# Kernel tuning notes

Measured on AMD Instinct MI355X. Metric: run time of the kernel, lower is better.

## Reference

```python
import jax, jax.numpy as jnp
import numpy as np

N_NODES, N_EDGES, N_GRAPHS = 50000, 800000, 128
D_IN, D_DEG, D_H, D_OUT, MAX_DEG = 32, 32, 64, 32, 128
D0 = D_IN + D_DEG + 1  # 65 = node_input_dim
N_GIN = 5  # num_layers - 1


def setup_inputs() -> dict:
    key = jax.random.key(0)
    ks = jax.random.split(key, 20)
    lin = lambda k, i, o: (jax.random.normal(k, (i, o), jnp.float32) / np.sqrt(i)).astype(jnp.float32)
    inp = {
        "x": jax.random.normal(ks[0], (N_NODES, D_IN), jnp.float32),
        "edge_index": jax.random.randint(ks[1], (2, N_EDGES), 0, N_NODES, jnp.int32),
        "batch": jnp.sort(jax.random.randint(ks[2], (N_NODES,), 0, N_GRAPHS, jnp.int32)),
        "root_n_id": jax.random.randint(ks[3], (N_GRAPHS,), 0, N_NODES, jnp.int32),
        "deg_table": 0.1 * jax.random.normal(ks[4], (MAX_DEG + 1, D_DEG), jnp.float32),
        # GIN layer 0 MLP (input dim 65), layers 1..4 (input dim 64), each MLP has 2 linears
        "w1_0": lin(ks[5], D0, D_H), "b1_0": 0.01 * jax.random.normal(ks[6], (D_H,), jnp.float32),
        "w2_0": lin(ks[7], D_H, D_H), "b2_0": 0.01 * jax.random.normal(ks[8], (D_H,), jnp.float32),
        "w1_rest": jnp.stack([lin(jax.random.fold_in(ks[9], i), D_H, D_H) for i in range(N_GIN - 1)]),
        "b1_rest": 0.01 * jax.random.normal(ks[10], (N_GIN - 1, D_H), jnp.float32),
        "w2_rest": jnp.stack([lin(jax.random.fold_in(ks[11], i), D_H, D_H) for i in range(N_GIN - 1)]),
        "b2_rest": 0.01 * jax.random.normal(ks[12], (N_GIN - 1, D_H), jnp.float32),
        # 3 BatchNorms per GIN layer: MLP-hidden BN, ApplyNodeFunc BN, outer BN
        "bn_gamma": 1.0 + 0.1 * jax.random.normal(ks[13], (N_GIN, 3, D_H), jnp.float32),
        "bn_beta": 0.1 * jax.random.normal(ks[14], (N_GIN, 3, D_H), jnp.float32),
        # per-layer prediction heads (layer 0 sees raw n_feat of dim 65)
        "pred_w0": lin(ks[15], D0, D_OUT), "pred_b0": 0.01 * jax.random.normal(ks[16], (D_OUT,), jnp.float32),
        "pred_w_rest": jnp.stack([lin(jax.random.fold_in(ks[17], i), D_H, D_OUT) for i in range(N_GIN)]),
        "pred_b_rest": 0.01 * jax.random.normal(ks[18], (N_GIN, D_OUT), jnp.float32),
    }
    return inp


def _bn(h, g, b):
    # training-mode BatchNorm1d over the node axis (biased variance), eps=1e-5
    m = h.mean(axis=0)
    v = h.var(axis=0)
    return g * (h - m) * jax.lax.rsqrt(v + 1e-5) + b


def _forward(x, edge_index, batch, root_n_id, deg_table, w1_0, b1_0, w2_0, b2_0,
             w1_rest, b1_rest, w2_rest, b2_rest, bn_gamma, bn_beta,
             pred_w0, pred_b0, pred_w_rest, pred_b_rest):
    N = x.shape[0]
    G = root_n_id.shape[0]
    src, dst = edge_index[0], edge_index[1]

    # degree(edge_index[0]) clamped to max_degree, then embedded
    deg = jax.ops.segment_sum(jnp.ones_like(src), src, num_segments=N)
    deg = jnp.clip(deg, 0, deg_table.shape[0] - 1)
    ego = jnp.zeros((N, 1), x.dtype).at[root_n_id].set(1.0)
    h = jnp.concatenate([x, deg_table[deg], ego], axis=-1)  # [N, 65]

    w1s = [w1_0] + [w1_rest[i] for i in range(w1_rest.shape[0])]
    b1s = [b1_0] + [b1_rest[i] for i in range(b1_rest.shape[0])]
    w2s = [w2_0] + [w2_rest[i] for i in range(w2_rest.shape[0])]
    b2s = [b2_0] + [b2_rest[i] for i in range(b2_rest.shape[0])]

    hidden = [h]
    for l in range(len(w1s)):
        # GINConv, sum aggregation, eps = 0: (1+eps)*h + sum_{j in N(i)} h_j
        agg = jax.ops.segment_sum(h[src], dst, num_segments=N)  # [N, d]
        z = h + agg
        z = jax.nn.relu(_bn(z @ w1s[l] + b1s[l], bn_gamma[l, 0], bn_beta[l, 0]))  # MLP hidden
        z = z @ w2s[l] + b2s[l]                                                  # MLP out (linear)
        z = jax.nn.relu(_bn(z, bn_gamma[l, 1], bn_beta[l, 1]))                   # ApplyNodeFunc BN+ReLU
        z = jax.nn.relu(_bn(z, bn_gamma[l, 2], bn_beta[l, 2]))                   # outer BN+ReLU
        h = z
        hidden.append(h)

    pred_ws = [pred_w0] + [pred_w_rest[i] for i in range(pred_w_rest.shape[0])]
    pred_bs = [pred_b0] + [pred_b_rest[i] for i in range(pred_b_rest.shape[0])]
    score = jnp.zeros((G, pred_w0.shape[1]), x.dtype)
    for i, hi in enumerate(hidden):
        pooled = jax.ops.segment_sum(hi, batch, num_segments=G)  # global_add_pool
        score = score + pooled @ pred_ws[i] + pred_bs[i]         # dropout is identity in eval
    # F.normalize(p=2, eps=1e-5)
    nrm = jnp.maximum(jnp.linalg.norm(score, axis=-1, keepdims=True), 1e-5)
    return score / nrm


def reference(x, edge_index, batch, root_n_id, deg_table, w1_0, b1_0, w2_0, b2_0,
              w1_rest, b1_rest, w2_rest, b2_rest, bn_gamma, bn_beta,
              pred_w0, pred_b0, pred_w_rest, pred_b_rest):
    return _forward(x, edge_index, batch, root_n_id, deg_table, w1_0, b1_0, w2_0, b2_0,
                    w1_rest, b1_rest, w2_rest, b2_rest, bn_gamma, bn_beta,
                    pred_w0, pred_b0, pred_w_rest, pred_b_rest)
```

## Files before the change

### kernel.cpp

```cpp
#include <hip/hip_runtime.h>

#define PAD 8
#define NREP 16
#define CHUNK 64

#define BCAST(v, l) __uint_as_float(__builtin_amdgcn_readlane(__float_as_uint(v), (l)))

__global__ __launch_bounds__(256) void count_k(const int* __restrict__ src,
    const int* __restrict__ dst, int* __restrict__ deg, int* __restrict__ cnt, int E) {
  int e = blockIdx.x * 256 + threadIdx.x;
  if (e < E) {
    atomicAdd(&deg[src[e] * PAD], 1);
    atomicAdd(&cnt[dst[e] * PAD], 1);
  }
}

__global__ __launch_bounds__(256) void scan1_k(const int* __restrict__ cnt,
    int* __restrict__ off, int* __restrict__ bsum, int N) {
  __shared__ int s[256];
  int t = threadIdx.x;
  int i = blockIdx.x * 256 + t;
  int c = (i < N) ? cnt[i * PAD] : 0;
  s[t] = c;
  __syncthreads();
  for (int d = 1; d < 256; d <<= 1) {
    int v = (t >= d) ? s[t - d] : 0;
    __syncthreads();
    s[t] += v;
    __syncthreads();
  }
  if (i < N) off[i + 1] = s[t];
  if (t == 255) bsum[blockIdx.x] = s[255];
}

__global__ __launch_bounds__(256) void scan2_k(int* __restrict__ bsum, int NB) {
  __shared__ int s[256];
  int t = threadIdx.x;
  int c = (t < NB) ? bsum[t] : 0;
  s[t] = c;
  __syncthreads();
  for (int d = 1; d < 256; d <<= 1) {
    int v = (t >= d) ? s[t - d] : 0;
    __syncthreads();
    s[t] += v;
    __syncthreads();
  }
  if (t < NB) bsum[t] = s[t] - c;
}

__global__ __launch_bounds__(256) void scan3_k(int* __restrict__ off,
    const int* __restrict__ bsum, int N) {
  int i = blockIdx.x * 256 + threadIdx.x;
  if (i < N) off[i + 1] += bsum[blockIdx.x];
  if (i == 0) off[0] = 0;
}

__global__ __launch_bounds__(256) void fill_k(const int* __restrict__ src,
    const int* __restrict__ dst, const int* __restrict__ off,
    int* __restrict__ cnt, int* __restrict__ csr, int E) {
  int e = blockIdx.x * 256 + threadIdx.x;
  if (e < E) {
    int d = dst[e];
    int old = atomicSub(&cnt[d * PAD], 1);
    csr[off[d + 1] - old] = src[e];
  }
}

__global__ void root_k(const int* __restrict__ root, int* __restrict__ egof, int G) {
  int g = threadIdx.x;
  if (g < G) egof[root[g]] = 1;
}

__global__ __launch_bounds__(256) void h0_k(const float* __restrict__ x,
    const float* __restrict__ deg_table, const int* __restrict__ deg,
    const int* __restrict__ egof, const int* __restrict__ batch,
    float* __restrict__ h0, float* __restrict__ pool0, int N) {
  int w = threadIdx.x >> 6, f = threadIdx.x & 63;
  int base = blockIdx.x * CHUNK;
  int end = min(base + CHUNK, N);
  float accum = 0.0f, accum64 = 0.0f;
  int curg = -1;
  for (int n0 = base + w; n0 < end; n0 += 4) {
    int n = __builtin_amdgcn_readfirstlane(n0);
    float v;
    if (f < 32) {
      v = x[n * 32 + f];
    } else {
      int d = deg[n * PAD];
      if (d > 128) d = 128;
      v = deg_table[d * 32 + (f - 32)];
    }
    h0[(size_t)n * 72 + f] = v;
    float e = 0.0f;
    if (f == 0) {
      e = egof[n] ? 1.0f : 0.0f;
      h0[(size_t)n * 72 + 64] = e;
    }
    int g = batch[n];
    if (g != curg) {
      if (curg >= 0) {
        atomicAdd(&pool0[curg * 72 + f], accum);
        if (f == 0 && accum64 != 0.0f) atomicAdd(&pool0[curg * 72 + 64], accum64);
      }
      curg = g;
      accum = v;
      accum64 = e;
    } else {
      accum += v;
      accum64 += e;
    }
  }
  if (curg >= 0) {
    atomicAdd(&pool0[curg * 72 + f], accum);
    if (f == 0 && accum64 != 0.0f) atomicAdd(&pool0[curg * 72 + 64], accum64);
  }
}

template <int FEATS, int STRIDE>
__global__ __launch_bounds__(256) void layer1_k(const float* __restrict__ h,
    const int* __restrict__ off, const int* __restrict__ csr,
    const float* __restrict__ W1, const float* __restrict__ B1,
    float* __restrict__ z1, float* __restrict__ sums, int N) {
  __shared__ float Wsh[FEATS * 64];
  __shared__ float ls[256], lq[256];
  const int t = threadIdx.x;
  for (int i = t; i < FEATS * 64; i += 256) Wsh[i] = W1[i];
  __syncthreads();
  const int w = t >> 6, lane = t & 63;
  const float bj = B1[lane];
  float s = 0.0f, q = 0.0f;
  const int step = gridDim.x * 4;
  for (int n0 = blockIdx.x * 4 + w; n0 < N; n0 += step) {
    const int n = __builtin_amdgcn_readfirstlane(n0);
    const float* row = h + (size_t)n * STRIDE;
    float z = row[lane];
    float z64 = 0.0f;
    if (FEATS == 65) { if (lane == 0) z64 = row[64]; }
    const int k1 = off[n + 1];
    int k = off[n];
    for (; k + 8 <= k1; k += 8) {
      int i0 = csr[k], i1 = csr[k + 1], i2 = csr[k + 2], i3 = csr[k + 3];
      int i4 = csr[k + 4], i5 = csr[k + 5], i6 = csr[k + 6], i7 = csr[k + 7];
      const float* r0 = h + (size_t)i0 * STRIDE;
      const float* r1 = h + (size_t)i1 * STRIDE;
      const float* r2 = h + (size_t)i2 * STRIDE;
      const float* r3 = h + (size_t)i3 * STRIDE;
      const float* r4 = h + (size_t)i4 * STRIDE;
      const float* r5 = h + (size_t)i5 * STRIDE;
      const float* r6 = h + (size_t)i6 * STRIDE;
      const float* r7 = h + (size_t)i7 * STRIDE;
      float v0 = r0[lane], v1 = r1[lane], v2 = r2[lane], v3 = r3[lane];
      float v4 = r4[lane], v5 = r5[lane], v6 = r6[lane], v7 = r7[lane];
      if (FEATS == 65) {
        if (lane == 0)
          z64 += ((r0[64] + r1[64]) + (r2[64] + r3[64])) +
                 ((r4[64] + r5[64]) + (r6[64] + r7[64]));
      }
      z += ((v0 + v1) + (v2 + v3)) + ((v4 + v5) + (v6 + v7));
    }
    for (; k < k1; k++) {
      const float* r0 = h + (size_t)csr[k] * STRIDE;
      z += r0[lane];
      if (FEATS == 65) { if (lane == 0) z64 += r0[64]; }
    }
    float a0 = bj, a1 = 0.0f, a2 = 0.0f, a3 = 0.0f;
#pragma unroll
    for (int k2 = 0; k2 < 64; k2 += 4) {
      a0 += BCAST(z, k2) * Wsh[k2 * 64 + lane];
      a1 += BCAST(z, k2 + 1) * Wsh[(k2 + 1) * 64 + lane];
      a2 += BCAST(z, k2 + 2) * Wsh[(k2 + 2) * 64 + lane];
      a3 += BCAST(z, k2 + 3) * Wsh[(k2 + 3) * 64 + lane];
    }
    if (FEATS == 65) a0 += BCAST(z64, 0) * Wsh[64 * 64 + lane];
    float acc = (a0 + a1) + (a2 + a3);
    z1[(size_t)n * 64 + lane] = acc;
    s += acc;
    q += acc * acc;
  }
  ls[t] = s; lq[t] = q;
  __syncthreads();
  if (t < 64) {
    float a = ls[t] + ls[64 + t] + ls[128 + t] + ls[192 + t];
    atomicAdd(&sums[(blockIdx.x & (NREP - 1)) * 128 + t], a);
  } else if (t < 128) {
    int f = t - 64;
    float a = lq[f] + lq[64 + f] + lq[128 + f] + lq[192 + f];
    atomicAdd(&sums[(blockIdx.x & (NREP - 1)) * 128 + 64 + f], a);
  }
}

__global__ __launch_bounds__(256) void layer2_k(const float* __restrict__ z1,
    const float* __restrict__ W2, const float* __restrict__ B2,
    const float* __restrict__ sums0, const float* __restrict__ g0,
    const float* __restrict__ be0, float invN,
    float* __restrict__ z2, float* __restrict__ sums1, int N) {
  __shared__ float Wsh[64 * 64];
  __shared__ float redu[128];
  __shared__ float scs[64], shs[64];
  __shared__ float ls[256], lq[256];
  const int t = threadIdx.x;
  for (int i = t; i < 64 * 64; i += 256) Wsh[i] = W2[i];
  if (t < 128) {
    float a = 0.0f;
#pragma unroll
    for (int b = 0; b < NREP; b++) a += sums0[b * 128 + t];
    redu[t] = a;
  }
  __syncthreads();
  if (t < 64) {
    float m = redu[t] * invN;
    float var = redu[64 + t] * invN - m * m;
    float sc = g0[t] * rsqrtf(var + 1e-5f);
    scs[t] = sc;
    shs[t] = be0[t] - m * sc;
  }
  __syncthreads();
  const int w = t >> 6, lane = t & 63;
  const float sc = scs[lane], sh = shs[lane];
  const float bj = B2[lane];
  float s = 0.0f, q = 0.0f;
  const int step = gridDim.x * 4;
  for (int n0 = blockIdx.x * 4 + w; n0 < N; n0 += step) {
    const int n = __builtin_amdgcn_readfirstlane(n0);
    float v = z1[(size_t)n * 64 + lane];
    v = fmaxf(v * sc + sh, 0.0f);
    float a0 = bj, a1 = 0.0f, a2 = 0.0f, a3 = 0.0f;
#pragma unroll
    for (int k2 = 0; k2 < 64; k2 += 4) {
      a0 += BCAST(v, k2) * Wsh[k2 * 64 + lane];
      a1 += BCAST(v, k2 + 1) * Wsh[(k2 + 1) * 64 + lane];
      a2 += BCAST(v, k2 + 2) * Wsh[(k2 + 2) * 64 + lane];
      a3 += BCAST(v, k2 + 3) * Wsh[(k2 + 3) * 64 + lane];
    }
    float acc = (a0 + a1) + (a2 + a3);
    z2[(size_t)n * 64 + lane] = acc;
    s += acc;
    q += acc * acc;
  }
  ls[t] = s; lq[t] = q;
  __syncthreads();
  if (t < 64) {
    float a = ls[t] + ls[64 + t] + ls[128 + t] + ls[192 + t];
    atomicAdd(&sums1[(blockIdx.x & (NREP - 1)) * 128 + t], a);
  } else if (t < 128) {
    int f = t - 64;
    float a = lq[f] + lq[64 + f] + lq[128 + f] + lq[192 + f];
    atomicAdd(&sums1[(blockIdx.x & (NREP - 1)) * 128 + 64 + f], a);
  }
}

__global__ __launch_bounds__(256) void statsbn_k(const float* __restrict__ z2,
    const float* __restrict__ sums1, const float* __restrict__ g1,
    const float* __restrict__ be1, float invN, float* __restrict__ sums2, int N) {
  __shared__ float redu[128];
  __shared__ float scs[64], shs[64];
  __shared__ float ls[256], lq[256];
  int t = threadIdx.x;
  if (t < 128) {
    float a = 0.0f;
#pragma unroll
    for (int b = 0; b < NREP; b++) a += sums1[b * 128 + t];
    redu[t] = a;
  }
  __syncthreads();
  if (t < 64) {
    float m = redu[t] * invN;
    float var = redu[64 + t] * invN - m * m;
    float sc = g1[t] * rsqrtf(var + 1e-5f);
    scs[t] = sc;
    shs[t] = be1[t] - m * sc;
  }
  __syncthreads();
  int f = t & 63, r = t >> 6;
  float sc = scs[f], sh = shs[f];
  float s = 0.0f, q = 0.0f;
  for (int n = blockIdx.x * 4 + r; n < N; n += gridDim.x * 4) {
    float v = z2[(size_t)n * 64 + f];
    v = fmaxf(v * sc + sh, 0.0f);
    s += v;
    q += v * v;
  }
  ls[t] = s; lq[t] = q;
  __syncthreads();
  if (t < 64) {
    float a = ls[t] + ls[64 + t] + ls[128 + t] + ls[192 + t];
    atomicAdd(&sums2[(blockIdx.x & (NREP - 1)) * 128 + t], a);
  } else if (t < 128) {
    int ff = t - 64;
    float a = lq[ff] + lq[64 + ff] + lq[128 + ff] + lq[192 + ff];
    atomicAdd(&sums2[(blockIdx.x & (NREP - 1)) * 128 + 64 + ff], a);
  }
}

__global__ __launch_bounds__(256) void apply_k(const float* __restrict__ z2,
    const float* __restrict__ sums1, const float* __restrict__ g1, const float* __restrict__ be1,
    const float* __restrict__ sums2, const float* __restrict__ g2, const float* __restrict__ be2,
    float invN, const int* __restrict__ batch, float* __restrict__ hout,
    float* __restrict__ pool, int N, int writeH) {
  __shared__ float red1[128], red2[128];
  __shared__ float sc1s[64], sh1s[64], sc2s[64], sh2s[64];
  int t = threadIdx.x;
  if (t < 128) {
    float a = 0.0f, c = 0.0f;
#pragma unroll
    for (int b = 0; b < NREP; b++) { a += sums1[b * 128 + t]; c += sums2[b * 128 + t]; }
    red1[t] = a;
    red2[t] = c;
  }
  __syncthreads();
  if (t < 64) {
    float m = red1[t] * invN;
    float var = red1[64 + t] * invN - m * m;
    float sc = g1[t] * rsqrtf(var + 1e-5f);
    sc1s[t] = sc;
    sh1s[t] = be1[t] - m * sc;
    m = red2[t] * invN;
    var = red2[64 + t] * invN - m * m;
    sc = g2[t] * rsqrtf(var + 1e-5f);
    sc2s[t] = sc;
    sh2s[t] = be2[t] - m * sc;
  }
  __syncthreads();
  int w = t >> 6, f = t & 63;
  float sc1 = sc1s[f], sh1 = sh1s[f], sc2 = sc2s[f], sh2 = sh2s[f];
  int base = blockIdx.x * CHUNK;
  int end = min(base + CHUNK, N);
  float accum = 0.0f;
  int curg = -1;
  for (int n0 = base + w; n0 < end; n0 += 4) {
    int n = __builtin_amdgcn_readfirstlane(n0);
    float v = z2[(size_t)n * 64 + f];
    v = fmaxf(v * sc1 + sh1, 0.0f);
    v = fmaxf(v * sc2 + sh2, 0.0f);
    if (writeH) hout[(size_t)n * 64 + f] = v;
    int g = batch[n];
    if (g != curg) {
      if (curg >= 0) atomicAdd(&pool[curg * 64 + f], accum);
      curg = g;
      accum = v;
    } else {
      accum += v;
    }
  }
  if (curg >= 0) atomicAdd(&pool[curg * 64 + f], accum);
}

__global__ __launch_bounds__(64) void prednorm_k(const float* __restrict__ pool0,
    const float* __restrict__ pools, const float* __restrict__ pw0,
    const float* __restrict__ pb0, const float* __restrict__ pwr,
    const float* __restrict__ pbr, float* __restrict__ out, int G) {
  int g = blockIdx.x;
  int j = threadIdx.x;
  float acc = 0.0f;
  if (j < 32) {
    acc = pb0[j];
    for (int k = 0; k < 65; k++) acc += pool0[g * 72 + k] * pw0[k * 32 + j];
    for (int l = 0; l < 5; l++) {
      acc += pbr[l * 32 + j];
      const float* pl = pools + (size_t)l * G * 64 + (size_t)g * 64;
      const float* wl = pwr + (size_t)l * 64 * 32;
      for (int k = 0; k < 64; k++) acc += pl[k] * wl[k * 32 + j];
    }
  }
  float s = acc * acc;
  for (int o = 16; o > 0; o >>= 1) s += __shfl_xor(s, o);
  float nrm = fmaxf(sqrtf(s), 1e-5f);
  if (j < 32) out[g * 32 + j] = acc / nrm;
}

extern "C" void kernel_launch(void* const* d_in, const int* in_sizes, int n_in,
                              void* d_out, int out_size, void* d_ws, size_t ws_size,
                              hipStream_t stream) {
  (void)n_in; (void)out_size; (void)ws_size;
  const float* x          = (const float*)d_in[0];
  const int*   edge_index = (const int*)d_in[1];
  const int*   batch      = (const int*)d_in[2];
  const int*   root       = (const int*)d_in[3];
  const float* deg_table  = (const float*)d_in[4];
  const float* w1_0       = (const float*)d_in[5];
  const float* b1_0       = (const float*)d_in[6];
  const float* w2_0       = (const float*)d_in[7];
  const float* b2_0       = (const float*)d_in[8];
  const float* w1_rest    = (const float*)d_in[9];
  const float* b1_rest    = (const float*)d_in[10];
  const float* w2_rest    = (const float*)d_in[11];
  const float* b2_rest    = (const float*)d_in[12];
  const float* bn_gamma   = (const float*)d_in[13];
  const float* bn_beta    = (const float*)d_in[14];
  const float* pred_w0    = (const float*)d_in[15];
  const float* pred_b0    = (const float*)d_in[16];
  const float* pred_w_rest = (const float*)d_in[17];
  const float* pred_b_rest = (const float*)d_in[18];

  const int N = in_sizes[0] / 32;
  const int E = in_sizes[1] / 2;
  const int G = in_sizes[3];
  const int* src = edge_index;
  const int* dst = edge_index + E;
  const float invN = 1.0f / N;

  char* w = (char*)d_ws;
  auto alloc = [&](size_t bytes) {
    char* p = w;
    w += (bytes + 255) & ~(size_t)255;
    return p;
  };
  int* d_deg  = (int*)alloc((size_t)N * PAD * 4);
  int* d_cnt  = (int*)alloc((size_t)N * PAD * 4);
  int* d_egof = (int*)alloc((size_t)N * 4);
  char* zero_int_end = w;
  int* d_off  = (int*)alloc((size_t)(N + 1) * 4);
  int* d_bsum = (int*)alloc(256 * 4);
  int* d_csr  = (int*)alloc((size_t)E * 4);
  float* fsums = (float*)alloc((size_t)15 * NREP * 128 * 4);
  float* fpool = (float*)alloc((size_t)(G * 72 + 5 * G * 64) * 4);
  char* zero_f_end = w;
  float* fh0 = (float*)alloc((size_t)N * 72 * 4);
  float* fB1 = (float*)alloc((size_t)N * 64 * 4);
  float* fB2 = (float*)alloc((size_t)N * 64 * 4);
  float* fB3 = (float*)alloc((size_t)N * 64 * 4);

  hipMemsetAsync(d_deg, 0, (size_t)(zero_int_end - (char*)d_deg), stream);
  hipMemsetAsync(fsums, 0, (size_t)(zero_f_end - (char*)fsums), stream);

  const int ebl = (E + 255) / 256;
  const int nb  = (N + 255) / 256;
  const int ncb = (N + CHUNK - 1) / CHUNK;

  count_k<<<ebl, 256, 0, stream>>>(src, dst, d_deg, d_cnt, E);
  scan1_k<<<nb, 256, 0, stream>>>(d_cnt, d_off, d_bsum, N);
  scan2_k<<<1, 256, 0, stream>>>(d_bsum, nb);
  scan3_k<<<nb, 256, 0, stream>>>(d_off, d_bsum, N);
  fill_k<<<ebl, 256, 0, stream>>>(src, dst, d_off, d_cnt, d_csr, E);
  root_k<<<1, 256, 0, stream>>>(root, d_egof, G);
  h0_k<<<ncb, 256, 0, stream>>>(x, deg_table, d_deg, d_egof, batch, fh0, fpool, N);

  float* pools = fpool + G * 72;
  const float* hcur = fh0;
  float* hnext = fB3;
  for (int l = 0; l < 5; l++) {
    const float* w1 = (l == 0) ? w1_0 : w1_rest + (size_t)(l - 1) * 64 * 64;
    const float* b1 = (l == 0) ? b1_0 : b1_rest + (size_t)(l - 1) * 64;
    const float* w2 = (l == 0) ? w2_0 : w2_rest + (size_t)(l - 1) * 64 * 64;
    const float* b2 = (l == 0) ? b2_0 : b2_rest + (size_t)(l - 1) * 64;
    float* sums0 = fsums + (size_t)(l * 3 + 0) * NREP * 128;
    float* sums1 = fsums + (size_t)(l * 3 + 1) * NREP * 128;
    float* sums2 = fsums + (size_t)(l * 3 + 2) * NREP * 128;
    const float* g0 = bn_gamma + (l * 3 + 0) * 64;
    const float* be0 = bn_beta + (l * 3 + 0) * 64;
    const float* g1 = bn_gamma + (l * 3 + 1) * 64;
    const float* be1 = bn_beta + (l * 3 + 1) * 64;
    const float* g2 = bn_gamma + (l * 3 + 2) * 64;
    const float* be2 = bn_beta + (l * 3 + 2) * 64;

    if (l == 0)
      layer1_k<65, 72><<<2048, 256, 0, stream>>>(hcur, d_off, d_csr, w1, b1, fB1, sums0, N);
    else
      layer1_k<64, 64><<<2048, 256, 0, stream>>>(hcur, d_off, d_csr, w1, b1, fB1, sums0, N);
    layer2_k<<<2048, 256, 0, stream>>>(fB1, w2, b2, sums0, g0, be0, invN, fB2, sums1, N);
    statsbn_k<<<1024, 256, 0, stream>>>(fB2, sums1, g1, be1, invN, sums2, N);
    float* pool_l = pools + (size_t)l * G * 64;
    apply_k<<<ncb, 256, 0, stream>>>(fB2, sums1, g1, be1, sums2, g2, be2, invN,
                                     batch, hnext, pool_l, N, (l < 4) ? 1 : 0);
    const float* tmp = hcur;
    hcur = hnext;
    hnext = (float*)tmp;
  }
  prednorm_k<<<G, 64, 0, stream>>>(fpool, pools, pred_w0, pred_b0,
                                   pred_w_rest, pred_b_rest, (float*)d_out, G);
}
```

Before: 670.8 us.

## Pair nodes per wave in gather, enlarge blocks, and merge setup kernels

```diff
diff --git a/kernel.cpp b/kernel.cpp
--- a/kernel.cpp
+++ b/kernel.cpp
@@ -33,9 +33,11 @@
   if (t == 255) bsum[blockIdx.x] = s[255];
 }
 
-__global__ __launch_bounds__(256) void scan2_k(int* __restrict__ bsum, int NB) {
+__global__ __launch_bounds__(256) void scan2root_k(int* __restrict__ bsum, int NB,
+    const int* __restrict__ root, int* __restrict__ egof, int G) {
   __shared__ int s[256];
   int t = threadIdx.x;
+  if (t < G) egof[root[t]] = 1;
   int c = (t < NB) ? bsum[t] : 0;
   s[t] = c;
   __syncthreads();
@@ -55,28 +57,24 @@
   if (i == 0) off[0] = 0;
 }
 
-__global__ __launch_bounds__(256) void fill_k(const int* __restrict__ src,
-    const int* __restrict__ dst, const int* __restrict__ off,
-    int* __restrict__ cnt, int* __restrict__ csr, int E) {
-  int e = blockIdx.x * 256 + threadIdx.x;
-  if (e < E) {
-    int d = dst[e];
-    int old = atomicSub(&cnt[d * PAD], 1);
-    csr[off[d + 1] - old] = src[e];
-  }
-}
-
-__global__ void root_k(const int* __restrict__ root, int* __restrict__ egof, int G) {
-  int g = threadIdx.x;
-  if (g < G) egof[root[g]] = 1;
-}
-
-__global__ __launch_bounds__(256) void h0_k(const float* __restrict__ x,
+__global__ __launch_bounds__(256) void fillh0_k(const int* __restrict__ src,
+    const int* __restrict__ dst, const int* __restrict__ off, int* __restrict__ cnt,
+    int* __restrict__ csr, int E, const float* __restrict__ x,
     const float* __restrict__ deg_table, const int* __restrict__ deg,
     const int* __restrict__ egof, const int* __restrict__ batch,
-    float* __restrict__ h0, float* __restrict__ pool0, int N) {
+    float* __restrict__ h0, float* __restrict__ pool0, int N, int ebl) {
+  if ((int)blockIdx.x < ebl) {
+    int e = blockIdx.x * 256 + threadIdx.x;
+    if (e < E) {
+      int d = dst[e];
+      int old = atomicSub(&cnt[d * PAD], 1);
+      csr[off[d + 1] - old] = src[e];
+    }
+    return;
+  }
+  int bid = blockIdx.x - ebl;
   int w = threadIdx.x >> 6, f = threadIdx.x & 63;
-  int base = blockIdx.x * CHUNK;
+  int base = bid * CHUNK;
   int end = min(base + CHUNK, N);
   float accum = 0.0f, accum64 = 0.0f;
   int curg = -1;
@@ -117,79 +115,147 @@
 }
 
 template <int FEATS, int STRIDE>
-__global__ __launch_bounds__(256) void layer1_k(const float* __restrict__ h,
+__global__ __launch_bounds__(512, 6) void layer1_k(const float* __restrict__ h,
     const int* __restrict__ off, const int* __restrict__ csr,
     const float* __restrict__ W1, const float* __restrict__ B1,
     float* __restrict__ z1, float* __restrict__ sums, int N) {
   __shared__ float Wsh[FEATS * 64];
-  __shared__ float ls[256], lq[256];
+  __shared__ float ls[512], lq[512];
   const int t = threadIdx.x;
-  for (int i = t; i < FEATS * 64; i += 256) Wsh[i] = W1[i];
+  for (int i = t; i < FEATS * 64; i += 512) Wsh[i] = W1[i];
   __syncthreads();
   const int w = t >> 6, lane = t & 63;
   const float bj = B1[lane];
   float s = 0.0f, q = 0.0f;
-  const int step = gridDim.x * 4;
-  for (int n0 = blockIdx.x * 4 + w; n0 < N; n0 += step) {
-    const int n = __builtin_amdgcn_readfirstlane(n0);
-    const float* row = h + (size_t)n * STRIDE;
-    float z = row[lane];
-    float z64 = 0.0f;
-    if (FEATS == 65) { if (lane == 0) z64 = row[64]; }
-    const int k1 = off[n + 1];
-    int k = off[n];
-    for (; k + 8 <= k1; k += 8) {
-      int i0 = csr[k], i1 = csr[k + 1], i2 = csr[k + 2], i3 = csr[k + 3];
-      int i4 = csr[k + 4], i5 = csr[k + 5], i6 = csr[k + 6], i7 = csr[k + 7];
-      const float* r0 = h + (size_t)i0 * STRIDE;
-      const float* r1 = h + (size_t)i1 * STRIDE;
-      const float* r2 = h + (size_t)i2 * STRIDE;
-      const float* r3 = h + (size_t)i3 * STRIDE;
-      const float* r4 = h + (size_t)i4 * STRIDE;
-      const float* r5 = h + (size_t)i5 * STRIDE;
-      const float* r6 = h + (size_t)i6 * STRIDE;
-      const float* r7 = h + (size_t)i7 * STRIDE;
-      float v0 = r0[lane], v1 = r1[lane], v2 = r2[lane], v3 = r3[lane];
-      float v4 = r4[lane], v5 = r5[lane], v6 = r6[lane], v7 = r7[lane];
+  const int step = gridDim.x * 16;
+  for (int n0 = blockIdx.x * 16 + w * 2; n0 < N; n0 += step) {
+    const int nA = __builtin_amdgcn_readfirstlane(n0);
+    const int nB = nA + 1;
+    const bool hasB = (nB < N);
+    const float* rowA = h + (size_t)nA * STRIDE;
+    float zA = rowA[lane], zB = 0.0f, zA64 = 0.0f, zB64 = 0.0f;
+    if (FEATS == 65) { if (lane == 0) zA64 = rowA[64]; }
+    int kA = off[nA];
+    const int k1A = off[nA + 1];
+    int kB = 0, k1B = 0;
+    if (hasB) {
+      const float* rowB = h + (size_t)nB * STRIDE;
+      zB = rowB[lane];
+      if (FEATS == 65) { if (lane == 0) zB64 = rowB[64]; }
+      kB = k1A;
+      k1B = off[nB + 1];
+    }
+    while (k1A - kA >= 4 && k1B - kB >= 4) {
+      int a0 = csr[kA], a1 = csr[kA + 1], a2 = csr[kA + 2], a3 = csr[kA + 3];
+      int b0 = csr[kB], b1 = csr[kB + 1], b2 = csr[kB + 2], b3 = csr[kB + 3];
+      const float* rA0 = h + (size_t)a0 * STRIDE;
+      const float* rA1 = h + (size_t)a1 * STRIDE;
+      const float* rA2 = h + (size_t)a2 * STRIDE;
+      const float* rA3 = h + (size_t)a3 * STRIDE;
+      const float* rB0 = h + (size_t)b0 * STRIDE;
+      const float* rB1 = h + (size_t)b1 * STRIDE;
+      const float* rB2 = h + (size_t)b2 * STRIDE;
+      const float* rB3 = h + (size_t)b3 * STRIDE;
+      float vA0 = rA0[lane], vA1 = rA1[lane], vA2 = rA2[lane], vA3 = rA3[lane];
+      float vB0 = rB0[lane], vB1 = rB1[lane], vB2 = rB2[lane], vB3 = rB3[lane];
       if (FEATS == 65) {
-        if (lane == 0)
-          z64 += ((r0[64] + r1[64]) + (r2[64] + r3[64])) +
-                 ((r4[64] + r5[64]) + (r6[64] + r7[64]));
+        if (lane == 0) {
+          zA64 += (rA0[64] + rA1[64]) + (rA2[64] + rA3[64]);
+          zB64 += (rB0[64] + rB1[64]) + (rB2[64] + rB3[64]);
+        }
       }
-      z += ((v0 + v1) + (v2 + v3)) + ((v4 + v5) + (v6 + v7));
-    }
-    for (; k < k1; k++) {
-      const float* r0 = h + (size_t)csr[k] * STRIDE;
-      z += r0[lane];
-      if (FEATS == 65) { if (lane == 0) z64 += r0[64]; }
-    }
-    float a0 = bj, a1 = 0.0f, a2 = 0.0f, a3 = 0.0f;
-#pragma unroll
-    for (int k2 = 0; k2 < 64; k2 += 4) {
-      a0 += BCAST(z, k2) * Wsh[k2 * 64 + lane];
-      a1 += BCAST(z, k2 + 1) * Wsh[(k2 + 1) * 64 + lane];
-      a2 += BCAST(z, k2 + 2) * Wsh[(k2 + 2) * 64 + lane];
-      a3 += BCAST(z, k2 + 3) * Wsh[(k2 + 3) * 64 + lane];
-    }
-    if (FEATS == 65) a0 += BCAST(z64, 0) * Wsh[64 * 64 + lane];
-    float acc = (a0 + a1) + (a2 + a3);
-    z1[(size_t)n * 64 + lane] = acc;
-    s += acc;
-    q += acc * acc;
-  }
-  ls[t] = s; lq[t] = q;
+      zA += (vA0 + vA1) + (vA2 + vA3);
+      zB += (vB0 + vB1) + (vB2 + vB3);
+      kA += 4;
+      kB += 4;
+    }
+    while (k1A - kA >= 4) {
+      int a0 = csr[kA], a1 = csr[kA + 1], a2 = csr[kA + 2], a3 = csr[kA + 3];
+      const float* rA0 = h + (size_t)a0 * STRIDE;
+      const float* rA1 = h + (size_t)a1 * STRIDE;
+      const float* rA2 = h + (size_t)a2 * STRIDE;
+      const float* rA3 = h + (size_t)a3 * STRIDE;
+      float vA0 = rA0[lane], vA1 = rA1[lane], vA2 = rA2[lane], vA3 = rA3[lane];
+      if (FEATS == 65) {
+        if (lane == 0) zA64 += (rA0[64] + rA1[64]) + (rA2[64] + rA3[64]);
+      }
+      zA += (vA0 + vA1) + (vA2 + vA3);
+      kA += 4;
+    }
+    while (kA < k1A) {
+      const float* r0 = h + (size_t)csr[kA] * STRIDE;
+      zA += r0[lane];
+      if (FEATS == 65) { if (lane == 0) zA64 += r0[64]; }
+      kA++;
+    }
+    while (k1B - kB >= 4) {
+      int b0 = csr[kB], b1 = csr[kB + 1], b2 = csr[kB + 2], b3 = csr[kB + 3];
+      const float* rB0 = h + (size_t)b0 * STRIDE;
+      const float* rB1 = h + (size_t)b1 * STRIDE;
+      const float* rB2 = h + (size_t)b2 * STRIDE;
+      const float* rB3 = h + (size_t)b3 * STRIDE;
+      float vB0 = rB0[lane], vB1 = rB1[lane], vB2 = rB2[lane], vB3 = rB3[lane];
+      if (FEATS == 65) {
+        if (lane == 0) zB64 += (rB0[64] + rB1[64]) + (rB2[64] + rB3[64]);
+      }
+      zB += (vB0 + vB1) + (vB2 + vB3);
+      kB += 4;
+    }
+    while (kB < k1B) {
+      const float* r0 = h + (size_t)csr[kB] * STRIDE;
+      zB += r0[lane];
+      if (FEATS == 65) { if (lane == 0) zB64 += r0[64]; }
+      kB++;
+    }
+    {
+      float a0 = bj, a1 = 0.0f, a2 = 0.0f, a3 = 0.0f;
+#pragma unroll
+      for (int k2 = 0; k2 < 64; k2 += 4) {
+        a0 += BCAST(zA, k2) * Wsh[k2 * 64 + lane];
+        a1 += BCAST(zA, k2 + 1) * Wsh[(k2 + 1) * 64 + lane];
+        a2 += BCAST(zA, k2 + 2) * Wsh[(k2 + 2) * 64 + lane];
+        a3 += BCAST(zA, k2 + 3) * Wsh[(k2 + 3) * 64 + lane];
+      }
+      if (FEATS == 65) a0 += BCAST(zA64, 0) * Wsh[64 * 64 + lane];
+      float acc = (a0 + a1) + (a2 + a3);
+      z1[(size_t)nA * 64 + lane] = acc;
+      s += acc;
+      q += acc * acc;
+    }
+    if (hasB) {
+      float a0 = bj, a1 = 0.0f, a2 = 0.0f, a3 = 0.0f;
+#pragma unroll
+      for (int k2 = 0; k2 < 64; k2 += 4) {
+        a0 += BCAST(zB, k2) * Wsh[k2 * 64 + lane];
+        a1 += BCAST(zB, k2 + 1) * Wsh[(k2 + 1) * 64 + lane];
+        a2 += BCAST(zB, k2 + 2) * Wsh[(k2 + 2) * 64 + lane];
+        a3 += BCAST(zB, k2 + 3) * Wsh[(k2 + 3) * 64 + lane];
+      }
+      if (FEATS == 65) a0 += BCAST(zB64, 0) * Wsh[64 * 64 + lane];
+      float acc = (a0 + a1) + (a2 + a3);
+      z1[(size_t)nB * 64 + lane] = acc;
+      s += acc;
+      q += acc * acc;
+    }
+  }
+  ls[t] = s;
+  lq[t] = q;
   __syncthreads();
   if (t < 64) {
-    float a = ls[t] + ls[64 + t] + ls[128 + t] + ls[192 + t];
+    float a = 0.0f;
+#pragma unroll
+    for (int r = 0; r < 8; r++) a += ls[r * 64 + t];
     atomicAdd(&sums[(blockIdx.x & (NREP - 1)) * 128 + t], a);
   } else if (t < 128) {
     int f = t - 64;
-    float a = lq[f] + lq[64 + f] + lq[128 + f] + lq[192 + f];
+    float a = 0.0f;
+#pragma unroll
+    for (int r = 0; r < 8; r++) a += lq[r * 64 + f];
     atomicAdd(&sums[(blockIdx.x & (NREP - 1)) * 128 + 64 + f], a);
   }
 }
 
-__global__ __launch_bounds__(256) void layer2_k(const float* __restrict__ z1,
+__global__ __launch_bounds__(512, 8) void layer2_k(const float* __restrict__ z1,
     const float* __restrict__ W2, const float* __restrict__ B2,
     const float* __restrict__ sums0, const float* __restrict__ g0,
     const float* __restrict__ be0, float invN,
@@ -197,9 +263,9 @@
   __shared__ float Wsh[64 * 64];
   __shared__ float redu[128];
   __shared__ float scs[64], shs[64];
-  __shared__ float ls[256], lq[256];
+  __shared__ float ls[512], lq[512];
   const int t = threadIdx.x;
-  for (int i = t; i < 64 * 64; i += 256) Wsh[i] = W2[i];
+  for (int i = t; i < 64 * 64; i += 512) Wsh[i] = W2[i];
   if (t < 128) {
     float a = 0.0f;
 #pragma unroll
@@ -219,8 +285,8 @@
   const float sc = scs[lane], sh = shs[lane];
   const float bj = B2[lane];
   float s = 0.0f, q = 0.0f;
-  const int step = gridDim.x * 4;
-  for (int n0 = blockIdx.x * 4 + w; n0 < N; n0 += step) {
+  const int step = gridDim.x * 8;
+  for (int n0 = blockIdx.x * 8 + w; n0 < N; n0 += step) {
     const int n = __builtin_amdgcn_readfirstlane(n0);
     float v = z1[(size_t)n * 64 + lane];
     v = fmaxf(v * sc + sh, 0.0f);
@@ -237,24 +303,29 @@
     s += acc;
     q += acc * acc;
   }
-  ls[t] = s; lq[t] = q;
+  ls[t] = s;
+  lq[t] = q;
   __syncthreads();
   if (t < 64) {
-    float a = ls[t] + ls[64 + t] + ls[128 + t] + ls[192 + t];
+    float a = 0.0f;
+#pragma unroll
+    for (int r = 0; r < 8; r++) a += ls[r * 64 + t];
     atomicAdd(&sums1[(blockIdx.x & (NREP - 1)) * 128 + t], a);
   } else if (t < 128) {
     int f = t - 64;
-    float a = lq[f] + lq[64 + f] + lq[128 + f] + lq[192 + f];
+    float a = 0.0f;
+#pragma unroll
+    for (int r = 0; r < 8; r++) a += lq[r * 64 + f];
     atomicAdd(&sums1[(blockIdx.x & (NREP - 1)) * 128 + 64 + f], a);
   }
 }
 
-__global__ __launch_bounds__(256) void statsbn_k(const float* __restrict__ z2,
+__global__ __launch_bounds__(1024, 8) void statsbn_k(const float* __restrict__ z2,
     const float* __restrict__ sums1, const float* __restrict__ g1,
     const float* __restrict__ be1, float invN, float* __restrict__ sums2, int N) {
   __shared__ float redu[128];
   __shared__ float scs[64], shs[64];
-  __shared__ float ls[256], lq[256];
+  __shared__ float ls[1024], lq[1024];
   int t = threadIdx.x;
   if (t < 128) {
     float a = 0.0f;
@@ -274,20 +345,25 @@
   int f = t & 63, r = t >> 6;
   float sc = scs[f], sh = shs[f];
   float s = 0.0f, q = 0.0f;
-  for (int n = blockIdx.x * 4 + r; n < N; n += gridDim.x * 4) {
+  for (int n = blockIdx.x * 16 + r; n < N; n += gridDim.x * 16) {
     float v = z2[(size_t)n * 64 + f];
     v = fmaxf(v * sc + sh, 0.0f);
     s += v;
     q += v * v;
   }
-  ls[t] = s; lq[t] = q;
+  ls[t] = s;
+  lq[t] = q;
   __syncthreads();
   if (t < 64) {
-    float a = ls[t] + ls[64 + t] + ls[128 + t] + ls[192 + t];
+    float a = 0.0f;
+#pragma unroll
+    for (int rr = 0; rr < 16; rr++) a += ls[rr * 64 + t];
     atomicAdd(&sums2[(blockIdx.x & (NREP - 1)) * 128 + t], a);
   } else if (t < 128) {
     int ff = t - 64;
-    float a = lq[ff] + lq[64 + ff] + lq[128 + ff] + lq[192 + ff];
+    float a = 0.0f;
+#pragma unroll
+    for (int rr = 0; rr < 16; rr++) a += lq[rr * 64 + ff];
     atomicAdd(&sums2[(blockIdx.x & (NREP - 1)) * 128 + 64 + ff], a);
   }
 }
@@ -429,11 +505,10 @@
 
   count_k<<<ebl, 256, 0, stream>>>(src, dst, d_deg, d_cnt, E);
   scan1_k<<<nb, 256, 0, stream>>>(d_cnt, d_off, d_bsum, N);
-  scan2_k<<<1, 256, 0, stream>>>(d_bsum, nb);
+  scan2root_k<<<1, 256, 0, stream>>>(d_bsum, nb, root, d_egof, G);
   scan3_k<<<nb, 256, 0, stream>>>(d_off, d_bsum, N);
-  fill_k<<<ebl, 256, 0, stream>>>(src, dst, d_off, d_cnt, d_csr, E);
-  root_k<<<1, 256, 0, stream>>>(root, d_egof, G);
-  h0_k<<<ncb, 256, 0, stream>>>(x, deg_table, d_deg, d_egof, batch, fh0, fpool, N);
+  fillh0_k<<<ebl + ncb, 256, 0, stream>>>(src, dst, d_off, d_cnt, d_csr, E,
+      x, deg_table, d_deg, d_egof, batch, fh0, fpool, N, ebl);
 
   float* pools = fpool + G * 72;
   const float* hcur = fh0;
@@ -454,11 +529,11 @@
     const float* be2 = bn_beta + (l * 3 + 2) * 64;
 
     if (l == 0)
-      layer1_k<65, 72><<<2048, 256, 0, stream>>>(hcur, d_off, d_csr, w1, b1, fB1, sums0, N);
+      layer1_k<65, 72><<<1024, 512, 0, stream>>>(hcur, d_off, d_csr, w1, b1, fB1, sums0, N);
     else
-      layer1_k<64, 64><<<2048, 256, 0, stream>>>(hcur, d_off, d_csr, w1, b1, fB1, sums0, N);
-    layer2_k<<<2048, 256, 0, stream>>>(fB1, w2, b2, sums0, g0, be0, invN, fB2, sums1, N);
-    statsbn_k<<<1024, 256, 0, stream>>>(fB2, sums1, g1, be1, invN, sums2, N);
+      layer1_k<64, 64><<<1024, 512, 0, stream>>>(hcur, d_off, d_csr, w1, b1, fB1, sums0, N);
+    layer2_k<<<1024, 512, 0, stream>>>(fB1, w2, b2, sums0, g0, be0, invN, fB2, sums1, N);
+    statsbn_k<<<512, 1024, 0, stream>>>(fB2, sums1, g1, be1, invN, sums2, N);
     float* pool_l = pools + (size_t)l * G * 64;
     apply_k<<<ncb, 256, 0, stream>>>(fB2, sums1, g1, be1, sums2, g2, be2, invN,
                                      batch, hnext, pool_l, N, (l < 4) ? 1 : 0);
```

New measurement: 1.056 ms. 57.5% more time.
